# Kernel tuning notes

Hardware: AMD Instinct MI355X
Metric: run time of the kernel (lower is better)

Reference implementation:

```python
import jax, jax.numpy as jnp
import numpy as np

B, N, M, QD, CD, H, DH = 4, 4096, 1024, 1024, 768, 8, 64
INNER = H * DH
SCALE = DH ** -0.5


def setup_inputs() -> dict:
    key = jax.random.key(0)
    ks = jax.random.split(key, 7)
    s = 0.02  # init scale for weights
    return {
        "x": jax.random.normal(ks[0], (B, N, QD), jnp.float32),
        "context": jax.random.normal(ks[1], (B, M, CD), jnp.float32),
        "Wq": jax.random.normal(ks[2], (QD, INNER), jnp.float32) * s,   # to_q (no bias)
        "Wk": jax.random.normal(ks[3], (CD, INNER), jnp.float32) * s,   # to_k (no bias)
        "Wv": jax.random.normal(ks[4], (CD, INNER), jnp.float32) * s,   # to_v (no bias)
        "Wo": jax.random.normal(ks[5], (INNER, QD), jnp.float32) * s,   # to_out[0] weight
        "bo": jnp.zeros((QD,), jnp.float32),                             # to_out[0] bias
    }


def reference(x, context, Wq, Wk, Wv, Wo, bo):
    # Standard cross-attention path of CrossAttention.forward
    # (context given, no injected Q_c/K_s/V_s, mask=None, dropout=0 -> identity).
    b, n, _ = x.shape
    m = context.shape[1]
    # b n (h d) -> b h n d
    q = (x @ Wq).reshape(b, n, H, DH).transpose(0, 2, 1, 3)
    k = (context @ Wk).reshape(b, m, H, DH).transpose(0, 2, 1, 3)
    v = (context @ Wv).reshape(b, m, H, DH).transpose(0, 2, 1, 3)
    sim = jnp.einsum('bhid,bhjd->bhij', q, k) * SCALE  # [b,h,n,m]
    attn = jax.nn.softmax(sim, axis=-1)
    out = jnp.einsum('bhij,bhjd->bhid', attn, v)       # [b,h,n,d]
    out = out.transpose(0, 2, 1, 3).reshape(b, n, INNER)
    return out @ Wo + bo                                # [b,n,query_dim]
```

## Files before the change

### kernel.cpp

```cpp
#include <hip/hip_runtime.h>
#include <cstdint>
#include <cstddef>

typedef unsigned short u16;
typedef __attribute__((ext_vector_type(8))) __bf16 bf16x8;
typedef __attribute__((ext_vector_type(4))) float f32x4;
typedef __attribute__((ext_vector_type(4))) uint32_t u32x4;

#define B_ 4
#define N_ 4096
#define M_ 1024
#define QD_ 1024
#define CD_ 768
#define H_ 8
#define DH_ 64
#define INNER_ 512

__device__ __forceinline__ u16 f2bf(float f) {
  uint32_t u = __builtin_bit_cast(uint32_t, f);
  u += 0x7fffu + ((u >> 16) & 1u);
  return (u16)(u >> 16);
}

__device__ __forceinline__ uint32_t pk2bf(float a, float b) {
#if __has_builtin(__builtin_amdgcn_cvt_pk_bf16_f32)
  typedef __attribute__((ext_vector_type(2))) __bf16 bf16x2;
  bf16x2 r = __builtin_amdgcn_cvt_pk_bf16_f32(a, b);
  return __builtin_bit_cast(uint32_t, r);
#elif __has_builtin(__builtin_amdgcn_perm)
  uint32_t ua = __builtin_bit_cast(uint32_t, a) + 0x8000u;
  uint32_t ub = __builtin_bit_cast(uint32_t, b) + 0x8000u;
  return __builtin_amdgcn_perm(ub, ua, 0x07060302u);
#else
  return (uint32_t)f2bf(a) | ((uint32_t)f2bf(b) << 16);
#endif
}

__device__ __forceinline__ void load_lds_16B(const void* g, void* l) {
  __builtin_amdgcn_global_load_lds(
      (__attribute__((address_space(1))) void*)(void*)g,
      (__attribute__((address_space(3))) void*)l, 16, 0, 0);
}

__device__ __forceinline__ bf16x8 ldfrag(const u16* p) {
  return __builtin_bit_cast(bf16x8, *(const uint4*)p);
}

__device__ __forceinline__ uint4 pk8(float4 a, float4 b) {
  uint4 p;
  p.x = pk2bf(a.x, a.y); p.y = pk2bf(a.z, a.w);
  p.z = pk2bf(b.x, b.y); p.w = pk2bf(b.z, b.w);
  return p;
}

__global__ __launch_bounds__(256) void transpose_all(const float* __restrict__ Wq,
                                                     const float* __restrict__ Wk,
                                                     const float* __restrict__ Wv,
                                                     const float* __restrict__ Wo,
                                                     u16* __restrict__ wqT,
                                                     u16* __restrict__ wkvT,
                                                     u16* __restrict__ woT,
                                                     float cl2) {
  __shared__ float tile[32][33];
  const int bid = blockIdx.x;
  const float* in; u16* out; int R, C; float scale; int bx, by;
  if (bid < 512)       { int r = bid;        in = Wq; out = wqT;  R = 1024; C = 512;  scale = 1.f; bx = r & 15; by = r >> 4; }
  else if (bid < 896)  { int r = bid - 512;  in = Wk; out = wkvT; R = 768;  C = 512;  scale = cl2; bx = r & 15; by = r >> 4; }
  else if (bid < 1280) { int r = bid - 896;  in = Wv; out = wkvT + (size_t)512 * 768; R = 768; C = 512; scale = 1.f; bx = r & 15; by = r >> 4; }
  else                 { int r = bid - 1280; in = Wo; out = woT;  R = 512;  C = 1024; scale = 1.f; bx = r & 31; by = r >> 5; }
  int tx = threadIdx.x & 31, ty = threadIdx.x >> 5;
  int c0 = bx * 32, r0 = by * 32;
#pragma unroll
  for (int j = 0; j < 4; j++)
    tile[ty + j * 8][tx] = in[(size_t)(r0 + ty + j * 8) * C + c0 + tx];
  __syncthreads();
#pragma unroll
  for (int j = 0; j < 4; j++)
    out[(size_t)(c0 + ty + j * 8) * R + r0 + tx] = f2bf(tile[tx][ty + j * 8] * scale);
}

__global__ __launch_bounds__(256) void gemm_bt_f32a(const float* __restrict__ A,
                                                    const u16* __restrict__ Bt,
                                                    u16* __restrict__ Cout,
                                                    int M, int N, int K,
                                                    u16* __restrict__ Kc) {
  __shared__ u16 As[2][128 * 32];
  __shared__ u16 Bs[2][128 * 32];
  const int t = threadIdx.x;
  const int nwg = gridDim.x * gridDim.y;
  const int lin = blockIdx.y * gridDim.x + blockIdx.x;
  const int chunk = nwg >> 3;
  const int swz = (lin & 7) * chunk + (lin >> 3);
  const int bx = swz % gridDim.x, by = swz / gridDim.x;
  const int m0 = by * 128, n0 = bx * 128;
  const int w = t >> 6, l = t & 63, lr = l & 15, qd = l >> 4;
  const int wm = (w >> 1) * 64, wn = (w & 1) * 64;
  f32x4 acc[4][4] = {};
  const float* gaf = A + (size_t)(m0 + (t >> 2)) * K + (t & 3) * 8;
  const u16* gb = Bt + (size_t)(n0 + (t >> 2)) * K + (t & 3) * 8;

  {
    float4 a0 = *(const float4*)(gaf);
    float4 a1 = *(const float4*)(gaf + 4);
    float4 b0 = *(const float4*)(gaf + (size_t)64 * K);
    float4 b1 = *(const float4*)(gaf + (size_t)64 * K + 4);
    load_lds_16B(gb, &Bs[0][t * 8]);
    load_lds_16B(gb + (size_t)64 * K, &Bs[0][t * 8 + 64 * 32]);
    *(uint4*)&As[0][t * 8] = pk8(a0, a1);
    *(uint4*)&As[0][t * 8 + 64 * 32] = pk8(b0, b1);
  }
  __syncthreads();

  const int NT = K >> 5;
  for (int kt = 0; kt < NT; kt++) {
    const int cur = kt & 1, nxt = cur ^ 1;
    float4 a0, a1, b0, b1;
    const bool pre = (kt + 1 < NT);
    if (pre) {
      const int kc = (kt + 1) * 32;
      a0 = *(const float4*)(gaf + kc);
      a1 = *(const float4*)(gaf + kc + 4);
      b0 = *(const float4*)(gaf + kc + (size_t)64 * K);
      b1 = *(const float4*)(gaf + kc + (size_t)64 * K + 4);
      load_lds_16B(gb + kc, &Bs[nxt][t * 8]);
      load_lds_16B(gb + kc + (size_t)64 * K, &Bs[nxt][t * 8 + 64 * 32]);
    }
    bf16x8 af[4], bf[4];
#pragma unroll
    for (int i = 0; i < 4; i++) af[i] = ldfrag(&As[cur][(wm + i * 16 + lr) * 32 + qd * 8]);
#pragma unroll
    for (int i = 0; i < 4; i++) bf[i] = ldfrag(&Bs[cur][(wn + i * 16 + lr) * 32 + qd * 8]);
#pragma unroll
    for (int mi = 0; mi < 4; mi++)
#pragma unroll
      for (int ni = 0; ni < 4; ni++)
        acc[mi][ni] = __builtin_amdgcn_mfma_f32_16x16x32_bf16(af[mi], bf[ni], acc[mi][ni], 0, 0, 0);
    if (pre) {
      *(uint4*)&As[nxt][t * 8] = pk8(a0, a1);
      *(uint4*)&As[nxt][t * 8 + 64 * 32] = pk8(b0, b1);
    }
    __syncthreads();
  }

  const bool kmode = (Kc != nullptr) && (n0 < 512);
  if (kmode) {
#pragma unroll
    for (int mi = 0; mi < 4; mi++)
#pragma unroll
      for (int ni = 0; ni < 4; ni++) {
        int col = n0 + wn + ni * 16 + lr;
        int h = col >> 6, c = (col >> 3) & 7, d0 = col & 7;
#pragma unroll
        for (int r = 0; r < 4; r++) {
          int row = m0 + wm + mi * 16 + qd * 4 + r;
          int b = row >> 10, m = row & 1023;
          int kt8 = m >> 7, ml = m & 127;
          size_t off = (size_t)((b << 3) + h) * 65536 + kt8 * 8192 + c * 1024 + ml * 8 + d0;
          Kc[off] = f2bf(acc[mi][ni][r]);
        }
      }
  } else {
#pragma unroll
    for (int mi = 0; mi < 4; mi++)
#pragma unroll
      for (int ni = 0; ni < 4; ni++) {
        int row = m0 + wm + mi * 16 + qd * 4;
        int col = n0 + wn + ni * 16 + lr;
#pragma unroll
        for (int r = 0; r < 4; r++)
          Cout[(size_t)(row + r) * N + col] = f2bf(acc[mi][ni][r]);
      }
  }
}

__global__ __launch_bounds__(512) void gemm256x128_bt(const u16* __restrict__ A,
                                                      const u16* __restrict__ Bt,
                                                      float* __restrict__ Cout,
                                                      int M, int N, int K,
                                                      const float* __restrict__ bias) {
  __shared__ u16 As[2][256 * 32];
  __shared__ u16 Bs[2][128 * 32];
  const int t = threadIdx.x;
  const int w = t >> 6, l = t & 63, lr = l & 15, qd = l >> 4;
  const int mw = w >> 1, nw2 = w & 1;
  const int nwg = gridDim.x * gridDim.y;
  const int lin = blockIdx.y * gridDim.x + blockIdx.x;
  const int chunk = nwg >> 3;
  const int swz = (lin & 7) * chunk + (lin >> 3);
  const int bx = swz % gridDim.x, by = swz / gridDim.x;
  const int m0 = by * 256, n0 = bx * 128;
  f32x4 acc[4][4] = {};
  const u16* ga = A + (size_t)(m0 + (t >> 2)) * K + (t & 3) * 8;
  const u16* gb = Bt + (size_t)(n0 + (t >> 2)) * K + (t & 3) * 8;

  load_lds_16B(ga, &As[0][t * 8]);
  load_lds_16B(ga + (size_t)128 * K, &As[0][(512 + t) * 8]);
  load_lds_16B(gb, &Bs[0][t * 8]);
  __syncthreads();

  const int NT = K >> 5;
  for (int kt = 0; kt < NT; kt++) {
    const int cur = kt & 1, nxt = cur ^ 1;
    if (kt + 1 < NT) {
      const int kc = (kt + 1) * 32;
      load_lds_16B(ga + kc, &As[nxt][t * 8]);
      load_lds_16B(ga + kc + (size_t)128 * K, &As[nxt][(512 + t) * 8]);
      load_lds_16B(gb + kc, &Bs[nxt][t * 8]);
    }
    bf16x8 af[4], bf[4];
#pragma unroll
    for (int i = 0; i < 4; i++) af[i] = ldfrag(&As[cur][(mw * 64 + i * 16 + lr) * 32 + qd * 8]);
#pragma unroll
    for (int j = 0; j < 4; j++) bf[j] = ldfrag(&Bs[cur][(nw2 * 64 + j * 16 + lr) * 32 + qd * 8]);
#pragma unroll
    for (int mi = 0; mi < 4; mi++)
#pragma unroll
      for (int ni = 0; ni < 4; ni++)
        acc[mi][ni] = __builtin_amdgcn_mfma_f32_16x16x32_bf16(af[mi], bf[ni], acc[mi][ni], 0, 0, 0);
    __syncthreads();
  }

#pragma unroll
  for (int mi = 0; mi < 4; mi++)
#pragma unroll
    for (int ni = 0; ni < 4; ni++) {
      int row = m0 + mw * 64 + mi * 16 + qd * 4;
      int col = n0 + nw2 * 64 + ni * 16 + lr;
#pragma unroll
      for (int r = 0; r < 4; r++)
        Cout[(size_t)(row + r) * N + col] = acc[mi][ni][r] + bias[col];
    }
}

__global__ __launch_bounds__(256) void repack_v(const u16* __restrict__ KVp,
                                                u16* __restrict__ Vtc) {
  int idx = blockIdx.x * 256 + threadIdx.x;
  int bh = idx >> 13, rest = idx & 8191;
  int kt = rest >> 10, sc = (rest >> 6) & 15, d = rest & 63;
  int b = bh >> 3, h = bh & 7;
  int g = sc >> 3, ksl = (sc >> 2) & 1, qd = sc & 3;
  ushort4 lo, hi;
  const u16* src = KVp + (size_t)(b * M_) * 1024 + 512 + h * 64 + d;
  int jb = kt * 128 + g * 64 + ksl * 16 + qd * 4;
  lo.x = src[(size_t)(jb + 0) * 1024];
  lo.y = src[(size_t)(jb + 1) * 1024];
  lo.z = src[(size_t)(jb + 2) * 1024];
  lo.w = src[(size_t)(jb + 3) * 1024];
  hi.x = src[(size_t)(jb + 32) * 1024];
  hi.y = src[(size_t)(jb + 33) * 1024];
  hi.z = src[(size_t)(jb + 34) * 1024];
  hi.w = src[(size_t)(jb + 35) * 1024];
  u16* dst = Vtc + (size_t)idx * 8;
  *(ushort4*)dst = lo;
  *(ushort4*)(dst + 4) = hi;
}

__global__ __launch_bounds__(256, 2) void attn_kernel(const u16* __restrict__ Qp,
                                                      const u16* __restrict__ Kc,
                                                      const u16* __restrict__ Vtc,
                                                      u16* __restrict__ Og) {
  __shared__ u16 Ks2[2][8192];
  __shared__ u16 Vts2[2][8192];
  const int t = threadIdx.x;
  const int w = t >> 6, l = t & 63, lr = l & 15, qd = l >> 4;
  const int nwg = gridDim.x * gridDim.y;
  const int lin = blockIdx.y * gridDim.x + blockIdx.x;
  const int chunk = nwg >> 3;
  const int swz = (lin & 7) * chunk + (lin >> 3);
  const int qt = swz % gridDim.x, bh = swz / gridDim.x;
  const int b = bh >> 3, h = bh & 7;

  const size_t qbase = ((size_t)(b * N_ + qt * 256 + w * 64)) * INNER_ + h * DH_;
  bf16x8 qf[4][2];
#pragma unroll
  for (int qt2 = 0; qt2 < 4; qt2++)
#pragma unroll
    for (int dh = 0; dh < 2; dh++)
      qf[qt2][dh] = __builtin_bit_cast(bf16x8,
          *(const uint4*)(Qp + qbase + (size_t)(qt2 * 16 + lr) * INNER_ + dh * 32 + qd * 8));

  f32x4 oacc[4][4] = {};
  f32x4 lacc[4] = {};
  const u16* ksrc0 = Kc + (size_t)bh * 65536;
  const u16* vsrc0 = Vtc + (size_t)bh * 65536;

  u32x4 onesw;
  onesw[0] = 0x3F803F80u; onesw[1] = 0x3F803F80u; onesw[2] = 0x3F803F80u; onesw[3] = 0x3F803F80u;
  const bf16x8 onesf = __builtin_bit_cast(bf16x8, onesw);

#pragma unroll
  for (int i = 0; i < 4; i++) load_lds_16B(ksrc0 + (i * 256 + t) * 8, &Ks2[0][(i * 256 + t) * 8]);
#pragma unroll
  for (int i = 0; i < 4; i++) load_lds_16B(vsrc0 + (i * 256 + t) * 8, &Vts2[0][(i * 256 + t) * 8]);
  __syncthreads();

  for (int kt = 0; kt < 8; kt++) {
    const int cur = kt & 1, nxt = cur ^ 1;
    if (kt < 7) {
      const u16* kn = ksrc0 + (kt + 1) * 8192;
      const u16* vn = vsrc0 + (kt + 1) * 8192;
#pragma unroll
      for (int i = 0; i < 4; i++) load_lds_16B(kn + (i * 256 + t) * 8, &Ks2[nxt][(i * 256 + t) * 8]);
#pragma unroll
      for (int i = 0; i < 4; i++) load_lds_16B(vn + (i * 256 + t) * 8, &Vts2[nxt][(i * 256 + t) * 8]);
    }
    const u16* Ksc = Ks2[cur];
    const u16* Vsc = Vts2[cur];

#pragma unroll
    for (int g = 0; g < 2; g++) {
      f32x4 sacc[4][4] = {};
#pragma unroll
      for (int jt = 0; jt < 4; jt++)
#pragma unroll
        for (int dh = 0; dh < 2; dh++) {
          bf16x8 kf = ldfrag(&Ksc[(dh * 4 + qd) * 1024 + (g * 64 + jt * 16 + lr) * 8]);
#pragma unroll
          for (int qt2 = 0; qt2 < 4; qt2++)
            sacc[jt][qt2] = __builtin_amdgcn_mfma_f32_16x16x32_bf16(kf, qf[qt2][dh], sacc[jt][qt2], 0, 0, 0);
        }
#pragma unroll
      for (int jt = 0; jt < 4; jt++)
#pragma unroll
        for (int qt2 = 0; qt2 < 4; qt2++)
#pragma unroll
          for (int r = 0; r < 4; r++)
            sacc[jt][qt2][r] = __builtin_amdgcn_exp2f(sacc[jt][qt2][r]);
      u32x4 pk[4][2];
#pragma unroll
      for (int qt2 = 0; qt2 < 4; qt2++)
#pragma unroll
        for (int ksl = 0; ksl < 2; ksl++)
#pragma unroll
          for (int v = 0; v < 4; v++) {
            int jt = (v >> 1) * 2 + ksl, r = (v & 1) * 2;
            pk[qt2][ksl][v] = pk2bf(sacc[jt][qt2][r], sacc[jt][qt2][r + 1]);
          }
#pragma unroll
      for (int ksl = 0; ksl < 2; ksl++) {
#pragma unroll
        for (int dt = 0; dt < 4; dt++) {
          bf16x8 vf = ldfrag(&Vsc[(g * 8 + ksl * 4 + qd) * 512 + (dt * 16 + lr) * 8]);
#pragma unroll
          for (int qt2 = 0; qt2 < 4; qt2++)
            oacc[qt2][dt] = __builtin_amdgcn_mfma_f32_16x16x32_bf16(
                vf, __builtin_bit_cast(bf16x8, pk[qt2][ksl]), oacc[qt2][dt], 0, 0, 0);
        }
#pragma unroll
        for (int qt2 = 0; qt2 < 4; qt2++)
          lacc[qt2] = __builtin_amdgcn_mfma_f32_16x16x32_bf16(
              onesf, __builtin_bit_cast(bf16x8, pk[qt2][ksl]), lacc[qt2], 0, 0, 0);
      }
    }
    __syncthreads();
  }

#pragma unroll
  for (int qt2 = 0; qt2 < 4; qt2++) {
    float inv = 1.f / lacc[qt2][0];
    int q = qt * 256 + w * 64 + qt2 * 16 + lr;
    size_t base = ((size_t)(b * N_ + q)) * INNER_ + h * DH_ + qd * 4;
#pragma unroll
    for (int dt = 0; dt < 4; dt++) {
      uint2 o;
      o.x = pk2bf(oacc[qt2][dt][0] * inv, oacc[qt2][dt][1] * inv);
      o.y = pk2bf(oacc[qt2][dt][2] * inv, oacc[qt2][dt][3] * inv);
      *(uint2*)(Og + base + dt * 16) = o;
    }
  }
}

extern "C" void kernel_launch(void* const* d_in, const int* in_sizes, int n_in,
                              void* d_out, int out_size, void* d_ws, size_t ws_size,
                              hipStream_t stream) {
  const float* x   = (const float*)d_in[0];
  const float* ctx = (const float*)d_in[1];
  const float* Wq  = (const float*)d_in[2];
  const float* Wk  = (const float*)d_in[3];
  const float* Wv  = (const float*)d_in[4];
  const float* Wo  = (const float*)d_in[5];
  const float* bo  = (const float*)d_in[6];
  float* out = (float*)d_out;

  const float cl2 = 0.18033688011112042f;

  u16* wqT  = (u16*)d_ws;
  u16* wkvT = wqT  + (size_t)512 * 1024;
  u16* woT  = wkvT + (size_t)1024 * 768;
  u16* Qp   = woT  + (size_t)1024 * 512;
  u16* Kc   = Qp   + (size_t)16384 * 512;
  u16* Vtc  = Kc   + (size_t)32 * 65536;
  u16* Og   = Vtc  + (size_t)32 * 65536;
  u16* KVp  = Og;

  transpose_all<<<1792, 256, 0, stream>>>(Wq, Wk, Wv, Wo, wqT, wkvT, woT, cl2);

  gemm_bt_f32a<<<dim3(4, 128), 256, 0, stream>>>(x, wqT, Qp, 16384, 512, 1024, nullptr);
  gemm_bt_f32a<<<dim3(8, 32), 256, 0, stream>>>(ctx, wkvT, KVp, 4096, 1024, 768, Kc);
  repack_v<<<1024, 256, 0, stream>>>(KVp, Vtc);

  attn_kernel<<<dim3(16, 32), 256, 0, stream>>>(Qp, Kc, Vtc, Og);

  gemm256x128_bt<<<dim3(8, 64), 512, 0, stream>>>(Og, woT, out, 16384, 1024, 512, bo);
}
```

Measured before the change: 263.5 us.

## Double K-tile depth in f32-A GEMM and add XOR-swizzled LDS layout

The projection GEMM now stages 64-wide K tiles instead of 32, which halves the number of barrier-separated iterations and issues more loads per stage. Tiles are stored in LDS with an XOR swizzle on 16-byte chunks (row & 7), with the same swizzle applied on the direct-to-LDS B loads and on fragment reads, to avoid bank conflicts from the wider row stride. The cost is double the LDS footprint (64 KB per block) and more registers for the staged A values, which can lower occupancy.

```diff
diff --git a/kernel.cpp b/kernel.cpp
--- a/kernel.cpp
+++ b/kernel.cpp
@@ -84,8 +84,8 @@
                                                     u16* __restrict__ Cout,
                                                     int M, int N, int K,
                                                     u16* __restrict__ Kc) {
-  __shared__ u16 As[2][128 * 32];
-  __shared__ u16 Bs[2][128 * 32];
+  __shared__ u16 As[2][128 * 64];
+  __shared__ u16 Bs[2][128 * 64];
   const int t = threadIdx.x;
   const int nwg = gridDim.x * gridDim.y;
   const int lin = blockIdx.y * gridDim.x + blockIdx.x;
@@ -96,48 +96,62 @@
   const int w = t >> 6, l = t & 63, lr = l & 15, qd = l >> 4;
   const int wm = (w >> 1) * 64, wn = (w & 1) * 64;
   f32x4 acc[4][4] = {};
-  const float* gaf = A + (size_t)(m0 + (t >> 2)) * K + (t & 3) * 8;
-  const u16* gb = Bt + (size_t)(n0 + (t >> 2)) * K + (t & 3) * 8;
+
+  const int srow[4] = { (t + 0) >> 3, (t + 256) >> 3, (t + 512) >> 3, (t + 768) >> 3 };
+  const int sc8 = t & 7;
+  const int lswz = sc8 ^ 0;
 
   {
-    float4 a0 = *(const float4*)(gaf);
-    float4 a1 = *(const float4*)(gaf + 4);
-    float4 b0 = *(const float4*)(gaf + (size_t)64 * K);
-    float4 b1 = *(const float4*)(gaf + (size_t)64 * K + 4);
-    load_lds_16B(gb, &Bs[0][t * 8]);
-    load_lds_16B(gb + (size_t)64 * K, &Bs[0][t * 8 + 64 * 32]);
-    *(uint4*)&As[0][t * 8] = pk8(a0, a1);
-    *(uint4*)&As[0][t * 8 + 64 * 32] = pk8(b0, b1);
+#pragma unroll
+    for (int i = 0; i < 4; i++) {
+      const int row = srow[i], c8 = sc8;
+      const float* s = A + (size_t)(m0 + row) * K + c8 * 8;
+      float4 a0 = *(const float4*)s;
+      float4 a1 = *(const float4*)(s + 4);
+      *(uint4*)&As[0][row * 64 + ((c8 ^ (row & 7)) * 8)] = pk8(a0, a1);
+      const int csrc = c8 ^ (row & 7);
+      load_lds_16B(Bt + (size_t)(n0 + row) * K + csrc * 8, &Bs[0][(t + i * 256) * 8]);
+    }
   }
   __syncthreads();
 
-  const int NT = K >> 5;
+  const int NT = K >> 6;
   for (int kt = 0; kt < NT; kt++) {
     const int cur = kt & 1, nxt = cur ^ 1;
-    float4 a0, a1, b0, b1;
+    float4 av0[4], av1[4];
     const bool pre = (kt + 1 < NT);
     if (pre) {
-      const int kc = (kt + 1) * 32;
-      a0 = *(const float4*)(gaf + kc);
-      a1 = *(const float4*)(gaf + kc + 4);
-      b0 = *(const float4*)(gaf + kc + (size_t)64 * K);
-      b1 = *(const float4*)(gaf + kc + (size_t)64 * K + 4);
-      load_lds_16B(gb + kc, &Bs[nxt][t * 8]);
-      load_lds_16B(gb + kc + (size_t)64 * K, &Bs[nxt][t * 8 + 64 * 32]);
-    }
-    bf16x8 af[4], bf[4];
-#pragma unroll
-    for (int i = 0; i < 4; i++) af[i] = ldfrag(&As[cur][(wm + i * 16 + lr) * 32 + qd * 8]);
-#pragma unroll
-    for (int i = 0; i < 4; i++) bf[i] = ldfrag(&Bs[cur][(wn + i * 16 + lr) * 32 + qd * 8]);
-#pragma unroll
-    for (int mi = 0; mi < 4; mi++)
-#pragma unroll
-      for (int ni = 0; ni < 4; ni++)
-        acc[mi][ni] = __builtin_amdgcn_mfma_f32_16x16x32_bf16(af[mi], bf[ni], acc[mi][ni], 0, 0, 0);
+      const int kc = (kt + 1) * 64;
+#pragma unroll
+      for (int i = 0; i < 4; i++) {
+        const int row = srow[i], c8 = sc8;
+        const float* s = A + (size_t)(m0 + row) * K + kc + c8 * 8;
+        av0[i] = *(const float4*)s;
+        av1[i] = *(const float4*)(s + 4);
+        const int csrc = c8 ^ (row & 7);
+        load_lds_16B(Bt + (size_t)(n0 + row) * K + kc + csrc * 8, &Bs[nxt][(t + i * 256) * 8]);
+      }
+    }
+#pragma unroll
+    for (int ks = 0; ks < 2; ks++) {
+      const int cs = ((ks * 4 + qd) ^ (lr & 7)) * 8;
+      bf16x8 af[4], bf[4];
+#pragma unroll
+      for (int i = 0; i < 4; i++) af[i] = ldfrag(&As[cur][(wm + i * 16 + lr) * 64 + cs]);
+#pragma unroll
+      for (int j = 0; j < 4; j++) bf[j] = ldfrag(&Bs[cur][(wn + j * 16 + lr) * 64 + cs]);
+#pragma unroll
+      for (int mi = 0; mi < 4; mi++)
+#pragma unroll
+        for (int ni = 0; ni < 4; ni++)
+          acc[mi][ni] = __builtin_amdgcn_mfma_f32_16x16x32_bf16(af[mi], bf[ni], acc[mi][ni], 0, 0, 0);
+    }
     if (pre) {
-      *(uint4*)&As[nxt][t * 8] = pk8(a0, a1);
-      *(uint4*)&As[nxt][t * 8 + 64 * 32] = pk8(b0, b1);
+#pragma unroll
+      for (int i = 0; i < 4; i++) {
+        const int row = srow[i], c8 = sc8;
+        *(uint4*)&As[nxt][row * 64 + ((c8 ^ (row & 7)) * 8)] = pk8(av0[i], av1[i]);
+      }
     }
     __syncthreads();
   }
```

Result: faster. 251.4 us (-4.6%).
